# Kernel optimization log

Measured on AMD Instinct MI355X. Metric: run time of the kernel, lower is better.

The kernel has to match this reference:

```python
import jax, jax.numpy as jnp
import numpy as np

M_HIST = 6
LAM = 1e-4
THRESHOLD = 50
BETA = 1.0


def _f_step(z, x, Wh, bh, Wx, bx, Wo, bo):
    # DEQ cell: f(z, x) = tanh(Linear(tanh(h_layer(x) + x_layer(z))))
    # (note: Func.forward(x, z) is called as f(z, x), so h_layer sees the
    #  external input x and x_layer sees the iterate z)
    hidden = jnp.tanh(x @ Wh.T + bh + z @ Wx.T + bx)  # [B,S,H]
    return jnp.tanh(hidden @ Wo.T + bo)               # [B,S,D]


def _anderson(f, x0):
    bsz = x0.shape[0]
    dL = x0.shape[1] * x0.shape[2]
    flat = lambda z: z.reshape(bsz, dL)
    unflat = lambda z: z.reshape(x0.shape)

    X = jnp.zeros((bsz, M_HIST, dL), dtype=x0.dtype)
    F = jnp.zeros((bsz, M_HIST, dL), dtype=x0.dtype)
    F0 = flat(f(x0))
    X = X.at[:, 0].set(flat(x0))
    F = F.at[:, 0].set(F0)
    X = X.at[:, 1].set(F0)
    F = F.at[:, 1].set(flat(f(unflat(F0))))

    lowest = jnp.asarray(1e8, dtype=x0.dtype)
    lowest_x = jnp.zeros((bsz, dL), dtype=x0.dtype)

    for k in range(2, THRESHOLD):  # fixed unrolled solver iterations
        n = min(k, M_HIST)
        G = F[:, :n] - X[:, :n]                       # [B,n,dL]
        GG = jnp.einsum('bnd,bmd->bnm', G, G) + LAM * jnp.eye(n, dtype=x0.dtype)
        H = jnp.zeros((bsz, n + 1, n + 1), dtype=x0.dtype)
        H = H.at[:, 0, 1:].set(1.0)
        H = H.at[:, 1:, 0].set(1.0)
        H = H.at[:, 1:, 1:].set(GG)
        rhs = jnp.zeros((bsz, n + 1, 1), dtype=x0.dtype).at[:, 0, 0].set(1.0)
        alpha = jnp.linalg.solve(H, rhs)[:, 1:, 0]    # [B,n]
        Xk = BETA * jnp.einsum('bn,bnd->bd', alpha, F[:, :n]) \
            + (1.0 - BETA) * jnp.einsum('bn,bnd->bd', alpha, X[:, :n])
        Fk = flat(f(unflat(Xk)))
        X = X.at[:, k % M_HIST].set(Xk)
        F = F.at[:, k % M_HIST].set(Fk)
        abs_diff = jnp.linalg.norm(Fk - Xk)
        rel_diff = abs_diff / (1e-5 + jnp.linalg.norm(Fk))
        better = rel_diff < lowest
        lowest_x = jnp.where(better, Xk, lowest_x)
        lowest = jnp.minimum(rel_diff, lowest)
    return unflat(lowest_x)


def setup_inputs() -> dict:
    key = jax.random.key(0)
    ks = jax.random.split(key, 9)
    B, S, D, H, O = 16384, 31, 14, 50, 1
    sc = lambda fan_in: 1.0 / np.sqrt(fan_in)
    return {
        'x':  jax.random.normal(ks[0], (B, S, D), jnp.float32),
        'Wh': jax.random.normal(ks[1], (H, D), jnp.float32) * sc(D),
        'bh': jax.random.normal(ks[2], (H,), jnp.float32) * sc(D),
        'Wx': jax.random.normal(ks[3], (H, D), jnp.float32) * sc(D),
        'bx': jax.random.normal(ks[4], (H,), jnp.float32) * sc(D),
        'Wo': jax.random.normal(ks[5], (D, H), jnp.float32) * sc(H),
        'bo': jax.random.normal(ks[6], (D,), jnp.float32) * sc(H),
        'Wf': jax.random.normal(ks[7], (O, S * D), jnp.float32) * sc(S * D),
        'bf': jax.random.normal(ks[8], (O,), jnp.float32) * sc(S * D),
    }


def reference(x, Wh, bh, Wx, bx, Wo, bo, Wf, bf):
    f = lambda z: _f_step(z, x, Wh, bh, Wx, bx, Wo, bo)
    z_star = _anderson(f, jnp.zeros_like(x))   # fixed-point solve (no grad)
    z = f(z_star)                              # one extra f application
    out = z.reshape(z.shape[0], -1) @ Wf.T + bf  # [B,1]
    return out
```

## Files before the change

kernel.cpp:

```cpp
#include <hip/hip_runtime.h>
#include <hip/hip_fp16.h>

#define S 31
#define D 14
#define H 50
#define NB 16384
#define NITER 48
#define LAMR 1e-4f
#define TSC 2.8853900817779268f

#define WS_D2   0
#define WS_F2   64
#define WS_WC1  128
#define WS_WOC  1152
#define WS_WF   1664
#define WS_OUTK 4096

typedef _Float16 f16x2 __attribute__((ext_vector_type(2)));
typedef _Float16 f16x4 __attribute__((ext_vector_type(4)));
typedef _Float16 f16x8 __attribute__((ext_vector_type(8)));
typedef float    f32x4 __attribute__((ext_vector_type(4)));

#if defined(__has_builtin) && __has_builtin(__builtin_amdgcn_rcpf)
#define FRCP(x) __builtin_amdgcn_rcpf(x)
#else
#define FRCP(x) (1.0f/(x))
#endif

#if defined(__has_builtin) && __has_builtin(__builtin_amdgcn_exp2f)
#define FEXP2(x) __builtin_amdgcn_exp2f(x)
#else
#define FEXP2(x) exp2f(x)
#endif

#define FDOT2(a,b,c) __builtin_amdgcn_fdot2((a),(b),(c),false)

__device__ __forceinline__ f16x2 pkrtz(float a, float b){
  auto r = __builtin_amdgcn_cvt_pkrtz(a, b);
  return __builtin_bit_cast(f16x2, r);
}

template<int CTRL>
__device__ __forceinline__ float dppadd(float v){
  int pv = __builtin_amdgcn_update_dpp(0, __builtin_bit_cast(int, v),
                                       CTRL, 0xF, 0xF, true);
  return v + __builtin_bit_cast(float, pv);
}

#define AIJ(i,j) ((i)*6 - ((i)*((i)+1))/2 + (j))

__device__ __forceinline__ float tfast(float x){
  float e = FEXP2(x);
  return 1.f - 2.f * FRCP(e + 1.f);
}

__global__ void prep_kernel(const float* __restrict__ Wh, const float* __restrict__ bh,
                            const float* __restrict__ Wx, const float* __restrict__ bx,
                            const float* __restrict__ Wo, const float* __restrict__ bo,
                            const float* __restrict__ Wf, float* __restrict__ ws){
  int t = threadIdx.x;
  for (int i=t;i<128;i+=256) ws[i]=0.f;
  __half2* wc1 = (__half2*)(ws + WS_WC1);
  for (int i=t;i<1024;i+=256){
    int n=i>>4, kp=i&15, k0=2*kp, k1=2*kp+1;
    float v0=0.f, v1=0.f;
    if (n<H){
      v0 = (k0<14)? Wh[n*D+k0]*TSC : (k0<28)? Wx[n*D+(k0-14)]*TSC : (k0==28)? (bh[n]+bx[n])*TSC : 0.f;
      v1 = (k1<14)? Wh[n*D+k1]*TSC : (k1<28)? Wx[n*D+(k1-14)]*TSC : (k1==28)? (bh[n]+bx[n])*TSC : 0.f;
    }
    wc1[i] = __floats2half2_rn(v0,v1);
  }
  __half2* woc = (__half2*)(ws + WS_WOC);
  for (int i=t;i<512;i+=256){
    int d=i>>5, kp=i&31, k0=2*kp, k1=2*kp+1;
    float v0=0.f, v1=0.f;
    if (d<D){
      v0 = (k0<H)? Wo[d*H+k0]*TSC : (k0==H)? bo[d]*TSC : 0.f;
      v1 = (k1<H)? Wo[d*H+k1]*TSC : (k1==H)? bo[d]*TSC : 0.f;
    }
    woc[i] = __floats2half2_rn(v0,v1);
  }
  __half2* wf = (__half2*)(ws + WS_WF);
  for (int i=t;i<256;i+=256){
    int s=i>>3, dp=i&7, d0=2*dp, d1=2*dp+1;
    float v0=(s<S&&d0<D)?Wf[s*D+d0]:0.f, v1=(s<S&&d1<D)?Wf[s*D+d1]:0.f;
    wf[i] = __floats2half2_rn(v0,v1);
  }
}

#define AZS 80
#define HBS 144
__global__ __launch_bounds__(64, 2)
void solver_kernel(const float* __restrict__ x,
                   const f16x8* __restrict__ wc1, const f16x8* __restrict__ woc,
                   const f16x2* __restrict__ wf,
                   float* __restrict__ outk, float* __restrict__ d2p, float* __restrict__ f2p){
  const int l = threadIdx.x;
  const int a = l & 15;
  const int g = l >> 4;
  const int elemA = blockIdx.x*2;

  __shared__ __align__(16) unsigned char AZ[64*AZS];
  __shared__ __align__(16) unsigned char HB[64*HBS];

#pragma unroll
  for (int i=0;i<20;++i) *(float*)(AZ + l*AZS + i*4) = 0.f;
  {
    int s = l & 31, e = l >> 5;
    if (s < S){
      const float* xr = x + ((size_t)(elemA+e)*S + s)*D;
#pragma unroll
      for (int i=0;i<7;++i){
        __half2 h2 = __floats2half2_rn(xr[2*i], xr[2*i+1]);
        *(f16x2*)(AZ + l*AZS + i*4) = __builtin_bit_cast(f16x2, h2);
      }
    }
    *(_Float16*)(AZ + l*AZS + 56) = (_Float16)1.0f;
  }
  const f16x8 wc1f0 = wc1[( 0+a)*4 + g], wc1f1 = wc1[(16+a)*4 + g];
  const f16x8 wc1f2 = wc1[(32+a)*4 + g], wc1f3 = wc1[(48+a)*4 + g];
  const f16x8 wA0 = woc[a*8 + g], wA1 = woc[a*8 + 4 + g];
  const f16x2 wfr0 = wf[a*8+g*2],      wfr1 = wf[a*8+g*2+1];
  const f16x2 wfr2 = wf[(16+a)*8+g*2], wfr3 = wf[(16+a)*8+g*2+1];

  const f16x2 zz = {(_Float16)0.f,(_Float16)0.f};
  const int zo0 = 28 + g*8;
  const int zo1 = (g==3) ? 60 : 32 + g*8;

  f16x2 Fh[48], Gh[48], fo[8];
  float GG[21];
#pragma unroll
  for (int i=0;i<48;++i){ Fh[i]=zz; Gh[i]=zz; }
#pragma unroll
  for (int i=0;i<21;++i) GG[i]=0.f;

#pragma unroll 1
  for (int kk=0; kk<50; ++kk){
    if (kk >= 2){
      float A_[21], yv[6];
      if (kk >= 6){
#pragma unroll
        for (int i=0;i<6;++i)
#pragma unroll
          for (int j=i;j<6;++j) A_[AIJ(i,j)] = GG[AIJ(i,j)] + ((i==j)?LAMR:0.f);
      } else {
        int lo = 6-kk;
#pragma unroll
        for (int i=0;i<6;++i)
#pragma unroll
          for (int j=i;j<6;++j){
            float v = GG[AIJ(i,j)] + ((i==j)?LAMR:0.f);
            A_[AIJ(i,j)] = (i>=lo)? v : ((i==j)?1e30f:0.f);
          }
      }
#pragma unroll
      for (int i=0;i<6;++i) yv[i]=1.f;
#pragma unroll
      for (int p=0;p<6;++p){
        float ip = FRCP(A_[AIJ(p,p)]);
        A_[AIJ(p,p)] = ip;
#pragma unroll
        for (int i=p+1;i<6;++i){
          float m = A_[AIJ(p,i)]*ip;
#pragma unroll
          for (int j=i;j<6;++j) A_[AIJ(i,j)] -= m*A_[AIJ(p,j)];
          yv[i] -= m*yv[p];
        }
      }
#pragma unroll
      for (int p=5;p>=0;--p){
        float acc=yv[p];
#pragma unroll
        for (int j=p+1;j<6;++j) acc -= A_[AIJ(p,j)]*yv[j];
        yv[p]=acc*A_[AIJ(p,p)];
      }
      float isum = FRCP(yv[0]+yv[1]+yv[2]+yv[3]+yv[4]+yv[5]);
      f16x2 xk[8];
#pragma unroll
      for (int i=0;i<8;++i) xk[i]=zz;
#pragma unroll
      for (int j=0;j<6;++j){
        float ao = yv[j]*isum;
        float ot = __shfl_xor(ao, 32);
        float vA = (l<32)? ao : ot;
        float vB = (l<32)? ot : ao;
        _Float16 hA=(_Float16)vA, hB=(_Float16)vB;
        f16x2 a2A={hA,hA}, a2B={hB,hB};
#pragma unroll
        for (int i=0;i<4;++i) xk[i] += a2A*Fh[j*8+i];
#pragma unroll
        for (int i=4;i<8;++i) xk[i] += a2B*Fh[j*8+i];
      }
#pragma unroll
      for (int nt=0;nt<4;++nt){
        int r = nt*16 + a;
        *(f16x2*)(AZ + r*AZS + zo0) = xk[nt*2];
        *(f16x2*)(AZ + r*AZS + zo1) = xk[nt*2+1];
      }
    } else if (kk == 1){
#pragma unroll
      for (int nt=0;nt<4;++nt){
        int r = nt*16 + a;
        *(f16x2*)(AZ + r*AZS + zo0) = fo[nt*2];
        *(f16x2*)(AZ + r*AZS + zo1) = fo[nt*2+1];
      }
    }
#pragma unroll
    for (int nt=0;nt<4;++nt){
      f16x8 B = *(const f16x8*)(AZ + (nt*16+a)*AZS + g*16);
#pragma unroll
      for (int mt=0;mt<4;++mt){
        f32x4 c = {0.f,0.f,0.f,0.f};
        f16x8 A = (mt==0)? wc1f0 : (mt==1)? wc1f1 : (mt==2)? wc1f2 : wc1f3;
        c = __builtin_amdgcn_mfma_f32_16x16x32_f16(A, B, c, 0,0,0);
        f16x4 hv;
#pragma unroll
        for (int q=0;q<4;++q){
          _Float16 t = (_Float16)tfast(c[q]);
          if (mt==3 && g==0 && q==2) t = (_Float16)1.0f;
          hv[q] = t;
        }
        *(f16x4*)(HB + (nt*16+a)*HBS + mt*32 + g*8) = hv;
      }
    }
#pragma unroll
    for (int nt=0;nt<4;++nt){
      int r2 = nt*16 + a;
      f16x8 b0 = *(const f16x8*)(HB + r2*HBS +  0 + g*16);
      f16x8 b1 = *(const f16x8*)(HB + r2*HBS + 64 + g*16);
      f32x4 c = {0.f,0.f,0.f,0.f};
      c = __builtin_amdgcn_mfma_f32_16x16x32_f16(wA0, b0, c, 0,0,0);
      c = __builtin_amdgcn_mfma_f32_16x16x32_f16(wA1, b1, c, 0,0,0);
      fo[nt*2]   = pkrtz(tfast(c[0]), tfast(c[1]));
      fo[nt*2+1] = pkrtz(tfast(c[2]), tfast(c[3]));
    }
    f16x2 go[8];
#pragma unroll
    for (int nt=0;nt<4;++nt){
      int r = nt*16 + a;
      f16x2 x0 = *(const f16x2*)(AZ + r*AZS + zo0);
      f16x2 x1 = *(const f16x2*)(AZ + r*AZS + zo1);
      go[nt*2]   = fo[nt*2]   - x0;
      go[nt*2+1] = fo[nt*2+1] - x1;
    }
    if (a == 15){
      fo[2]=zz; fo[3]=zz; fo[6]=zz; fo[7]=zz;
      go[2]=zz; go[3]=zz; go[6]=zz; go[7]=zz;
    }
#pragma unroll
    for (int j=0;j<5;++j)
#pragma unroll
      for (int i=0;i<8;++i){ Fh[j*8+i]=Fh[(j+1)*8+i]; Gh[j*8+i]=Gh[(j+1)*8+i]; }
#pragma unroll
    for (int i=0;i<8;++i){ Fh[40+i]=fo[i]; Gh[40+i]=go[i]; }
    float rv[16];
#pragma unroll
    for (int j=0;j<5;++j){
      float pa=0.f, pb=0.f;
#pragma unroll
      for (int i=0;i<4;++i) pa = FDOT2(Gh[40+i], Gh[j*8+i], pa);
#pragma unroll
      for (int i=4;i<8;++i) pb = FDOT2(Gh[40+i], Gh[j*8+i], pb);
      rv[j]=pa; rv[8+j]=pb;
    }
    {
      float pa=0.f,pb=0.f,qa=0.f,qb=0.f,ra=0.f,rb=0.f;
#pragma unroll
      for (int i=0;i<4;++i){
        pa = FDOT2(Gh[40+i], Gh[40+i], pa);
        qa = FDOT2(Fh[40+i], Fh[40+i], qa);
      }
#pragma unroll
      for (int i=4;i<8;++i){
        pb = FDOT2(Gh[40+i], Gh[40+i], pb);
        qb = FDOT2(Fh[40+i], Fh[40+i], qb);
      }
      ra = FDOT2(Fh[40+0], wfr0, ra); ra = FDOT2(Fh[40+1], wfr1, ra);
      ra = FDOT2(Fh[40+2], wfr2, ra); ra = FDOT2(Fh[40+3], wfr3, ra);
      rb = FDOT2(Fh[44+0], wfr0, rb); rb = FDOT2(Fh[44+1], wfr1, rb);
      rb = FDOT2(Fh[44+2], wfr2, rb); rb = FDOT2(Fh[44+3], wfr3, rb);
      rv[5]=pa; rv[13]=pb; rv[6]=qa; rv[14]=qb; rv[7]=ra; rv[15]=rb;
    }
#pragma unroll
    for (int i=0;i<16;++i) rv[i] = dppadd<0x121>(rv[i]);
#pragma unroll
    for (int i=0;i<16;++i) rv[i] = dppadd<0x122>(rv[i]);
#pragma unroll
    for (int i=0;i<16;++i) rv[i] = dppadd<0x124>(rv[i]);
#pragma unroll
    for (int i=0;i<16;++i) rv[i] = dppadd<0x128>(rv[i]);
#pragma unroll
    for (int i=0;i<16;++i) rv[i] += __shfl_xor(rv[i],16);
#pragma unroll
    for (int i=0;i<16;++i) rv[i] += __shfl_xor(rv[i],32);
    const bool eB = (l >= 32);
#pragma unroll
    for (int i_=0;i_<5;++i_)
#pragma unroll
      for (int j_=i_;j_<5;++j_) GG[AIJ(i_,j_)] = GG[AIJ(i_+1,j_+1)];
#pragma unroll
    for (int j=0;j<5;++j) GG[AIJ(j,5)] = eB? rv[8+j] : rv[j];
    GG[AIJ(5,5)] = eB? rv[13] : rv[5];
    if (kk>=2 && l==0){
      atomicAdd(&d2p[kk-2], rv[5]+rv[13]);
      atomicAdd(&f2p[kk-2], rv[6]+rv[14]);
      outk[(size_t)(kk-2)*NB + elemA]     = rv[7];
      outk[(size_t)(kk-2)*NB + elemA + 1] = rv[15];
    }
  }
}

__global__ void final_kernel(const float* __restrict__ d2p, const float* __restrict__ f2p,
                             const float* __restrict__ outk, const float* __restrict__ bf,
                             float* __restrict__ out){
  int b = blockIdx.x*blockDim.x + threadIdx.x;
  float best = 1e8f; int kst = 0;
  for (int k=0;k<NITER;++k){
    float rel = sqrtf(d2p[k]) / (1e-5f + sqrtf(f2p[k]));
    if (rel < best){ best = rel; kst = k; }
  }
  out[b] = outk[(size_t)kst*NB + b] + bf[0];
}

extern "C" void kernel_launch(void* const* d_in, const int* in_sizes, int n_in,
                              void* d_out, int out_size, void* d_ws, size_t ws_size,
                              hipStream_t stream){
  const float* x  = (const float*)d_in[0];
  const float* Wh = (const float*)d_in[1];
  const float* bh = (const float*)d_in[2];
  const float* Wx = (const float*)d_in[3];
  const float* bx = (const float*)d_in[4];
  const float* Wo = (const float*)d_in[5];
  const float* bo = (const float*)d_in[6];
  const float* Wf = (const float*)d_in[7];
  const float* bf = (const float*)d_in[8];
  float* ws  = (float*)d_ws;
  float* out = (float*)d_out;

  hipLaunchKernelGGL(prep_kernel, dim3(1), dim3(256), 0, stream, Wh,bh,Wx,bx,Wo,bo,Wf,ws);
  hipLaunchKernelGGL(solver_kernel, dim3(NB/2), dim3(64), 0, stream,
                     x, (const f16x8*)(ws+WS_WC1), (const f16x8*)(ws+WS_WOC),
                     (const f16x2*)(ws+WS_WF),
                     ws+WS_OUTK, ws+WS_D2, ws+WS_F2);
  hipLaunchKernelGGL(final_kernel, dim3(NB/256), dim3(256), 0, stream,
                     ws+WS_D2, ws+WS_F2, ws+WS_OUTK, bf, out);
}
```

Before: 2.909 ms.

## Build MFMA B operand from registers via shuffles instead of LDS staging

Removes the per-iteration LDS round trip (AZ buffer) used to assemble the first-layer MFMA B operand from the x input and the current iterate. The constant x/bias part is loaded once into registers (binv), and the iterate slots are filled each iteration through cross-lane shuffles. The residual G = F - X now uses register copies instead of re-reading LDS. It trades LDS stores, loads and waits for several shuffles and selects per tile, and adds register pressure under a 64-thread, 2-wave launch bound.

```diff
diff --git a/kernel.cpp b/kernel.cpp
--- a/kernel.cpp
+++ b/kernel.cpp
@@ -34,6 +34,8 @@
 #endif
 
 #define FDOT2(a,b,c) __builtin_amdgcn_fdot2((a),(b),(c),false)
+#define F2I(v) __builtin_bit_cast(int,(v))
+#define I2F(v) __builtin_bit_cast(float,(v))
 
 __device__ __forceinline__ f16x2 pkrtz(float a, float b){
   auto r = __builtin_amdgcn_cvt_pkrtz(a, b);
@@ -88,7 +90,6 @@
   }
 }
 
-#define AZS 80
 #define HBS 144
 __global__ __launch_bounds__(64, 2)
 void solver_kernel(const float* __restrict__ x,
@@ -100,11 +101,10 @@
   const int g = l >> 4;
   const int elemA = blockIdx.x*2;
 
-  __shared__ __align__(16) unsigned char AZ[64*AZS];
   __shared__ __align__(16) unsigned char HB[64*HBS];
 
 #pragma unroll
-  for (int i=0;i<20;++i) *(float*)(AZ + l*AZS + i*4) = 0.f;
+  for (int i=0;i<12;++i) *(float*)(HB + l*48 + i*4) = 0.f;
   {
     int s = l & 31, e = l >> 5;
     if (s < S){
@@ -112,10 +112,19 @@
 #pragma unroll
       for (int i=0;i<7;++i){
         __half2 h2 = __floats2half2_rn(xr[2*i], xr[2*i+1]);
-        *(f16x2*)(AZ + l*AZS + i*4) = __builtin_bit_cast(f16x2, h2);
-      }
-    }
-    *(_Float16*)(AZ + l*AZS + 56) = (_Float16)1.0f;
+        *(f16x2*)(HB + l*48 + i*4) = __builtin_bit_cast(f16x2, h2);
+      }
+    }
+  }
+  int4 binv[4];
+  {
+    int off = (g<3 ? g : 2)*16;
+#pragma unroll
+    for (int nt=0;nt<4;++nt){
+      int4 v = *(const int4*)(HB + (nt*16+a)*48 + off);
+      if (g==3) v.z = 0x00003C00;
+      binv[nt] = v;
+    }
   }
   const f16x8 wc1f0 = wc1[( 0+a)*4 + g], wc1f1 = wc1[(16+a)*4 + g];
   const f16x8 wc1f2 = wc1[(32+a)*4 + g], wc1f3 = wc1[(48+a)*4 + g];
@@ -124,13 +133,13 @@
   const f16x2 wfr2 = wf[(16+a)*8+g*2], wfr3 = wf[(16+a)*8+g*2+1];
 
   const f16x2 zz = {(_Float16)0.f,(_Float16)0.f};
-  const int zo0 = 28 + g*8;
-  const int zo1 = (g==3) ? 60 : 32 + g*8;
-
-  f16x2 Fh[48], Gh[48], fo[8];
+
+  f16x2 Fh[48], Gh[48], fo[8], xo[8];
   float GG[21];
 #pragma unroll
   for (int i=0;i<48;++i){ Fh[i]=zz; Gh[i]=zz; }
+#pragma unroll
+  for (int i=0;i<8;++i) xo[i]=zz;
 #pragma unroll
   for (int i=0;i<21;++i) GG[i]=0.f;
 
@@ -175,9 +184,8 @@
         yv[p]=acc*A_[AIJ(p,p)];
       }
       float isum = FRCP(yv[0]+yv[1]+yv[2]+yv[3]+yv[4]+yv[5]);
-      f16x2 xk[8];
-#pragma unroll
-      for (int i=0;i<8;++i) xk[i]=zz;
+#pragma unroll
+      for (int i=0;i<8;++i) xo[i]=zz;
 #pragma unroll
       for (int j=0;j<6;++j){
         float ao = yv[j]*isum;
@@ -187,32 +195,42 @@
         _Float16 hA=(_Float16)vA, hB=(_Float16)vB;
         f16x2 a2A={hA,hA}, a2B={hB,hB};
 #pragma unroll
-        for (int i=0;i<4;++i) xk[i] += a2A*Fh[j*8+i];
-#pragma unroll
-        for (int i=4;i<8;++i) xk[i] += a2B*Fh[j*8+i];
-      }
+        for (int i=0;i<4;++i) xo[i] += a2A*Fh[j*8+i];
+#pragma unroll
+        for (int i=4;i<8;++i) xo[i] += a2B*Fh[j*8+i];
+      }
+    } else if (kk == 1){
+#pragma unroll
+      for (int i=0;i<8;++i) xo[i]=fo[i];
+    }
+    f16x8 bz[4];
+    {
+      float xof[8];
+#pragma unroll
+      for (int i=0;i<8;++i) xof[i] = __builtin_bit_cast(float, xo[i]);
 #pragma unroll
       for (int nt=0;nt<4;++nt){
-        int r = nt*16 + a;
-        *(f16x2*)(AZ + r*AZS + zo0) = xk[nt*2];
-        *(f16x2*)(AZ + r*AZS + zo1) = xk[nt*2+1];
-      }
-    } else if (kk == 1){
-#pragma unroll
-      for (int nt=0;nt<4;++nt){
-        int r = nt*16 + a;
-        *(f16x2*)(AZ + r*AZS + zo0) = fo[nt*2];
-        *(f16x2*)(AZ + r*AZS + zo1) = fo[nt*2+1];
+        float t01 = __shfl(xof[nt*2],   a);
+        float t02 = __shfl(xof[nt*2+1], a);
+        float t12a= __shfl(xof[nt*2],   a+16);
+        float t12b= __shfl(xof[nt*2+1], a+16);
+        float t23 = __shfl(xof[nt*2+1], a+32);
+        int4 bv = binv[nt];
+        float dw0 = (g==2)? t02  : (g==3)? t23        : I2F(bv.x);
+        float dw1 = (g==2)? t12a : (g==3)? xof[nt*2]  : I2F(bv.y);
+        float dw2 = (g==2)? t12b :                      I2F(bv.z);
+        float dw3 = (g==1)? t01  : (g==2)? xof[nt*2]  : I2F(bv.w);
+        int4 bi = { F2I(dw0), F2I(dw1), F2I(dw2), F2I(dw3) };
+        bz[nt] = __builtin_bit_cast(f16x8, bi);
       }
     }
 #pragma unroll
     for (int nt=0;nt<4;++nt){
-      f16x8 B = *(const f16x8*)(AZ + (nt*16+a)*AZS + g*16);
 #pragma unroll
       for (int mt=0;mt<4;++mt){
         f32x4 c = {0.f,0.f,0.f,0.f};
         f16x8 A = (mt==0)? wc1f0 : (mt==1)? wc1f1 : (mt==2)? wc1f2 : wc1f3;
-        c = __builtin_amdgcn_mfma_f32_16x16x32_f16(A, B, c, 0,0,0);
+        c = __builtin_amdgcn_mfma_f32_16x16x32_f16(A, bz[nt], c, 0,0,0);
         f16x4 hv;
 #pragma unroll
         for (int q=0;q<4;++q){
@@ -236,13 +254,7 @@
     }
     f16x2 go[8];
 #pragma unroll
-    for (int nt=0;nt<4;++nt){
-      int r = nt*16 + a;
-      f16x2 x0 = *(const f16x2*)(AZ + r*AZS + zo0);
-      f16x2 x1 = *(const f16x2*)(AZ + r*AZS + zo1);
-      go[nt*2]   = fo[nt*2]   - x0;
-      go[nt*2+1] = fo[nt*2+1] - x1;
-    }
+    for (int i=0;i<8;++i) go[i] = fo[i] - xo[i];
     if (a == 15){
       fo[2]=zz; fo[3]=zz; fo[6]=zz; fo[7]=zz;
       go[2]=zz; go[3]=zz; go[6]=zz; go[7]=zz;
```

After: 2.995 ms. 3.0% more time.
